# Performance work log

Measured on AMD Instinct MI355X. Metric: run time of the kernel, lower is better.

The kernel has to match this reference:

```python
import jax, jax.numpy as jnp
import numpy as np

N_USERS = 100000
N_ITEMS = 50000
NNZ = 3000000  # user-item interactions; symmetric adjacency has 2*NNZ edges
D = 64
N_LAYERS = 3


def setup_inputs() -> dict:
    key = jax.random.key(0)
    k1, k2, k3 = jax.random.split(key, 3)
    N = N_USERS + N_ITEMS
    users = jax.random.randint(k1, (NNZ,), 0, N_USERS)
    items = jax.random.randint(k2, (NNZ,), 0, N_ITEMS) + N_USERS
    # symmetric bipartite adjacency: u->i and i->u edges
    row = jnp.concatenate([users, items]).astype(jnp.int32)
    col = jnp.concatenate([items, users]).astype(jnp.int32)
    # D^{-1/2} A D^{-1/2} normalization, matching (deg + 1e-7)^{-0.5}
    deg = jax.ops.segment_sum(jnp.ones(row.shape, dtype=jnp.float32), row, num_segments=N)
    dinv = jnp.power(deg + 1e-7, -0.5)
    vals = dinv[row] * dinv[col]
    in_embs = jax.random.normal(k3, (N, D), dtype=jnp.float32)
    return {"in_embs": in_embs, "row": row, "col": col, "vals": vals, "n_layers": N_LAYERS}


def reference(in_embs, row, col, vals, n_layers):
    N = in_embs.shape[0]
    # result = in_embs + sum_i [ x_i/(i+1) + x_i ]  (original appends both per layer)
    out = in_embs
    x = in_embs
    for i in range(n_layers):
        # SpMM: x <- A_norm @ x  via gather + segment scatter-add
        x = jax.ops.segment_sum(vals[:, None] * x[col], row, num_segments=N)
        # F.normalize(x, dim=-1) with torch's eps=1e-12 clamp
        x = x / jnp.maximum(jnp.linalg.norm(x, axis=-1, keepdims=True), 1e-12)
        out = out + x * (1.0 + 1.0 / (i + 1))
    return out
```

## Files before the change

kernel.cpp:

```cpp
#include <hip/hip_runtime.h>
#include <hip/hip_bf16.h>

#define D 64
#define BW 512
#define BSH 9
#define BMASK 511
#define MAXK 512
#define CHUNK 8192

typedef unsigned short u16;
typedef unsigned int u32;
typedef _Float16 half2_t __attribute__((ext_vector_type(2)));

__device__ __forceinline__ u16 f2h(float f) {
    union { _Float16 h; u16 u; } v; v.h = (_Float16)f; return v.u;
}
__device__ __forceinline__ float hlo(u32 u) {
    union { u32 x; half2_t h; } v; v.x = u; return (float)v.h.x;
}
__device__ __forceinline__ float hhi(u32 u) {
    union { u32 x; half2_t h; } v; v.x = u; return (float)v.h.y;
}
__device__ __forceinline__ float dot2lo(u32 u, float acc) {
    union { u32 x; half2_t h; } v; v.x = u;
    half2_t one = {(_Float16)1.0f, (_Float16)0.0f};
    return __builtin_amdgcn_fdot2(v.h, one, acc, false);
}
__device__ __forceinline__ float dot2hi(u32 u, float acc) {
    union { u32 x; half2_t h; } v; v.x = u;
    half2_t one = {(_Float16)0.0f, (_Float16)1.0f};
    return __builtin_amdgcn_fdot2(v.h, one, acc, false);
}


__global__ __launch_bounds__(256) void chunk_hist_kernel(
        const int* __restrict__ row, int* __restrict__ H,
        int E, int K, int nchunks) {
    __shared__ int h[MAXK];
    int ch = blockIdx.x;
    int cbeg = ch * CHUNK;
    int cend = min(cbeg + CHUNK, E);
    for (int i = threadIdx.x; i < K; i += 256) h[i] = 0;
    __syncthreads();
    for (int e = cbeg + threadIdx.x; e < cend; e += 256)
        atomicAdd(&h[row[e] >> BSH], 1);
    __syncthreads();
    for (int i = threadIdx.x; i < K; i += 256)
        H[(size_t)i * nchunks + ch] = h[i];
}


__global__ __launch_bounds__(256) void bucket_colscan_kernel(
        int* __restrict__ H, int* __restrict__ btot, int nchunks) {
    __shared__ int tmp[256];
    int b = blockIdx.x;
    int t = threadIdx.x;
    int* Hb = H + (size_t)b * nchunks;
    int cpt = (nchunks + 255) >> 8;
    int beg = min(t * cpt, nchunks), end = min(beg + cpt, nchunks);
    int s = 0;
    for (int i = beg; i < end; ++i) s += Hb[i];
    tmp[t] = s;
    __syncthreads();
    for (int d = 1; d < 256; d <<= 1) {
        int x = (t >= d) ? tmp[t - d] : 0;
        __syncthreads();
        tmp[t] += x;
        __syncthreads();
    }
    int run = tmp[t] - s;
    for (int i = beg; i < end; ++i) {
        int v = Hb[i];
        Hb[i] = run;
        run += v;
    }
    if (t == 255) btot[b] = tmp[255];
}


__global__ __launch_bounds__(1024) void bucket_scan_kernel(
        const int* __restrict__ btot, int* __restrict__ bbase, int K, int E) {
    __shared__ int tmp[1024];
    int t = threadIdx.x;
    int v = (t < K) ? btot[t] : 0;
    tmp[t] = v;
    __syncthreads();
    for (int d = 1; d < 1024; d <<= 1) {
        int x = (t >= d) ? tmp[t - d] : 0;
        __syncthreads();
        tmp[t] += x;
        __syncthreads();
    }
    if (t < K) bbase[t] = tmp[t] - v;
    if (t == 0) bbase[K] = E;
}


__global__ __launch_bounds__(256) void scatter_sort_kernel(
        const int* __restrict__ row, const int* __restrict__ col,
        const int* __restrict__ H, const int* __restrict__ btot,
        const int* __restrict__ bbase,
        u32* __restrict__ pairs, int E, int K, int nchunks) {
    __shared__ u32 stage[CHUNK];
    __shared__ int hcur[MAXK];
    __shared__ int lbase[MAXK + 1];
    __shared__ int gdest[MAXK];
    __shared__ int red[256];
    int ch = blockIdx.x;
    int cbeg = ch * CHUNK;
    int cend = min(cbeg + CHUNK, E);
    int cnt_total = cend - cbeg;
    int t = threadIdx.x;

    int c0 = 0, c1 = 0;
    int i0 = t, i1 = t + 256;
    if (i0 < K) {
        int st = H[(size_t)i0 * nchunks + ch];
        int en = (ch + 1 < nchunks) ? H[(size_t)i0 * nchunks + ch + 1] : btot[i0];
        c0 = en - st;
        gdest[i0] = bbase[i0] + st;
    }
    if (i1 < K) {
        int st = H[(size_t)i1 * nchunks + ch];
        int en = (ch + 1 < nchunks) ? H[(size_t)i1 * nchunks + ch + 1] : btot[i1];
        c1 = en - st;
        gdest[i1] = bbase[i1] + st;
    }
    __syncthreads();
    int j0 = 2 * t, j1 = 2 * t + 1;
    int d0 = 0, d1 = 0;
    if (j0 < K) {
        int st = H[(size_t)j0 * nchunks + ch];
        int en = (ch + 1 < nchunks) ? H[(size_t)j0 * nchunks + ch + 1] : btot[j0];
        d0 = en - st;
        gdest[j0] = bbase[j0] + st;
    }
    if (j1 < K) {
        int st = H[(size_t)j1 * nchunks + ch];
        int en = (ch + 1 < nchunks) ? H[(size_t)j1 * nchunks + ch + 1] : btot[j1];
        d1 = en - st;
        gdest[j1] = bbase[j1] + st;
    }
    int s = d0 + d1;
    red[t] = s;
    __syncthreads();
    for (int d = 1; d < 256; d <<= 1) {
        int x = (t >= d) ? red[t - d] : 0;
        __syncthreads();
        red[t] += x;
        __syncthreads();
    }
    int ex = red[t] - s;
    if (j0 < K) { lbase[j0] = ex; hcur[j0] = ex; }
    if (j1 < K) { lbase[j1] = ex + d0; hcur[j1] = ex + d0; }
    if (t == 255) lbase[K] = red[255];
    __syncthreads();

    for (int e = cbeg + t; e < cend; e += 256) {
        int r = row[e];
        u32 c = (u32)col[e];
        int p = atomicAdd(&hcur[r >> BSH], 1);
        stage[p] = ((u32)(r & BMASK) << 18) | c;
    }
    __syncthreads();

    for (int p = t; p < cnt_total; p += 256) {
        int lo = 0, hi = K;
        while (hi - lo > 1) {
            int mid = (lo + hi) >> 1;
            if (lbase[mid] <= p) lo = mid; else hi = mid;
        }
        pairs[gdest[lo] + (p - lbase[lo])] = stage[p];
    }
}


__global__ __launch_bounds__(256) void build_csr_kernel(
        const u32* __restrict__ pairs, const int* __restrict__ bbase,
        int* __restrict__ ptr, float* __restrict__ dinv,
        float* __restrict__ sdeg, int* __restrict__ ccol, int N, int K) {
    __shared__ int hd[BW];
    __shared__ int red[256];
    int k = blockIdx.x;
    int ebeg = bbase[k], eend = bbase[k + 1];
    int r0 = k << BSH;
    int t = threadIdx.x;
    hd[t] = 0;
    hd[t + 256] = 0;
    __syncthreads();
    for (int e = ebeg + t; e < eend; e += 256)
        atomicAdd(&hd[pairs[e] >> 18], 1);
    __syncthreads();
    int v0 = hd[2 * t], v1 = hd[2 * t + 1];
    int s = v0 + v1;
    red[t] = s;
    __syncthreads();
    for (int d = 1; d < 256; d <<= 1) {
        int x = (t >= d) ? red[t - d] : 0;
        __syncthreads();
        red[t] += x;
        __syncthreads();
    }
    int ex = red[t] - s;
    int fb0 = ebeg + ex;
    int fb1 = ebeg + ex + v0;
    int ra = r0 + 2 * t, rb = r0 + 2 * t + 1;
    if (ra < N) {
        ptr[ra] = fb0;
        float f = (float)v0 + 1e-7f;
        float sq = sqrtf(f);
        dinv[ra] = 1.0f / sq;
        sdeg[ra] = sq;
    }
    if (rb < N) {
        ptr[rb] = fb1;
        float f = (float)v1 + 1e-7f;
        float sq = sqrtf(f);
        dinv[rb] = 1.0f / sq;
        sdeg[rb] = sq;
    }
    hd[2 * t] = fb0;
    hd[2 * t + 1] = fb1;
    if (k == 0 && t == 0) ptr[N] = eend >= 0 ? bbase[K] : 0;
    __syncthreads();
    for (int e = ebeg + t; e < eend; e += 256) {
        u32 pk = pairs[e];
        int pos = atomicAdd(&hd[pk >> 18], 1);
        ccol[pos] = (int)(pk & 0x3FFFFu);
    }
}

__global__ void scale_in_kernel(const float* __restrict__ in,
                                const float* __restrict__ dinv,
                                u16* __restrict__ y0, int npairs) {
    int p = blockIdx.x * blockDim.x + threadIdx.x;
    if (p >= npairs) return;
    float2 v = *reinterpret_cast<const float2*>(&in[(size_t)p * 2]);
    float dv = dinv[p >> 5];
    u32 up = (u32)f2h(v.x * dv) | ((u32)f2h(v.y * dv) << 16);
    *reinterpret_cast<u32*>(&y0[(size_t)p * 2]) = up;
}

template <bool FINAL>
__global__ __launch_bounds__(256) void layer_kernel(
        const u16* __restrict__ y_src,
        const int* __restrict__ ptr,
        const int* __restrict__ ccol,
        const float* __restrict__ dinv,
        const float* __restrict__ sdeg,
        u16* __restrict__ y_dst,
        const float* __restrict__ in_embs,
        const u16* __restrict__ y1,
        float* __restrict__ out,
        int rbeg, int rend) {
    int wid = (blockIdx.x * blockDim.x + threadIdx.x) >> 6;
    int lane = threadIdx.x & 63;
    int rh = lane >> 5;
    int b = (lane >> 3) & 3;
    int a = lane & 7;
    int r = rbeg + wid * 2 + rh;
    if (r >= rend) return;
    const size_t dimoff = (size_t)a * 8;

    int s = ptr[r], e = ptr[r + 1];
    float acc[8];
    #pragma unroll
    for (int i = 0; i < 8; ++i) acc[i] = 0.f;

#define ACCQ(q)                                            \
    do {                                                   \
        u32 qa_[4] = {(q).x, (q).y, (q).z, (q).w};         \
        _Pragma("unroll")                                  \
        for (int i_ = 0; i_ < 4; ++i_) {                   \
            acc[2 * i_]     = dot2lo(qa_[i_], acc[2 * i_]);     \
            acc[2 * i_ + 1] = dot2hi(qa_[i_], acc[2 * i_ + 1]); \
        }                                                  \
    } while (0)

    int j = s;
    #pragma unroll 2
    for (; j + 8 <= e; j += 8) {
        int c0 = __builtin_nontemporal_load(&ccol[j + b]);
        int c1 = __builtin_nontemporal_load(&ccol[j + 4 + b]);
        uint4 q0 = *reinterpret_cast<const uint4*>(&y_src[(size_t)c0 * D + dimoff]);
        uint4 q1 = *reinterpret_cast<const uint4*>(&y_src[(size_t)c1 * D + dimoff]);
        ACCQ(q0);
        ACCQ(q1);
    }
    if (j + 4 <= e) {
        int c = __builtin_nontemporal_load(&ccol[j + b]);
        uint4 q = *reinterpret_cast<const uint4*>(&y_src[(size_t)c * D + dimoff]);
        ACCQ(q);
        j += 4;
    }
    if (j + b < e) {
        int c = __builtin_nontemporal_load(&ccol[j + b]);
        uint4 q = *reinterpret_cast<const uint4*>(&y_src[(size_t)c * D + dimoff]);
        ACCQ(q);
    }
#undef ACCQ

    #pragma unroll
    for (int off = 8; off <= 16; off <<= 1) {
        #pragma unroll
        for (int i = 0; i < 8; ++i) acc[i] += __shfl_xor(acc[i], off);
    }

    float ss = 0.f;
    #pragma unroll
    for (int i = 0; i < 8; ++i) ss += acc[i] * acc[i];
    #pragma unroll
    for (int off = 1; off <= 4; off <<= 1) ss += __shfl_xor(ss, off);
    float inv = 1.0f / fmaxf(sqrtf(ss), 1e-12f);

    if (b == 0) {
        size_t idx = (size_t)r * D + dimoff;
        if (FINAL) {
            float sd = sdeg[r];
            float4 i0 = *reinterpret_cast<const float4*>(&in_embs[idx]);
            float4 i1 = *reinterpret_cast<const float4*>(&in_embs[idx + 4]);
            uint4 w1 = *reinterpret_cast<const uint4*>(&y1[idx]);
            uint4 w2 = *reinterpret_cast<const uint4*>(&y_src[idx]);
            u32 w1a[4] = {w1.x, w1.y, w1.z, w1.w};
            u32 w2a[4] = {w2.x, w2.y, w2.z, w2.w};
            float o[8];
            #pragma unroll
            for (int i = 0; i < 4; ++i) {
                o[2 * i]     = 2.0f * sd * hlo(w1a[i]) + 1.5f * sd * hlo(w2a[i])
                             + (4.0f / 3.0f) * acc[2 * i] * inv;
                o[2 * i + 1] = 2.0f * sd * hhi(w1a[i]) + 1.5f * sd * hhi(w2a[i])
                             + (4.0f / 3.0f) * acc[2 * i + 1] * inv;
            }
            float4 o0 = {o[0] + i0.x, o[1] + i0.y, o[2] + i0.z, o[3] + i0.w};
            float4 o1 = {o[4] + i1.x, o[5] + i1.y, o[6] + i1.z, o[7] + i1.w};
            *reinterpret_cast<float4*>(&out[idx])     = o0;
            *reinterpret_cast<float4*>(&out[idx + 4]) = o1;
        } else {
            float dv = dinv[r] * inv;
            uint4 w;
            w.x = (u32)f2h(acc[0] * dv) | ((u32)f2h(acc[1] * dv) << 16);
            w.y = (u32)f2h(acc[2] * dv) | ((u32)f2h(acc[3] * dv) << 16);
            w.z = (u32)f2h(acc[4] * dv) | ((u32)f2h(acc[5] * dv) << 16);
            w.w = (u32)f2h(acc[6] * dv) | ((u32)f2h(acc[7] * dv) << 16);
            *reinterpret_cast<uint4*>(&y_dst[idx]) = w;
        }
    }
}


__global__ void spmm_scatter_kernel(const float* __restrict__ x_src,
                                    const int* __restrict__ row,
                                    const int* __restrict__ col,
                                    const float* __restrict__ vals,
                                    float* __restrict__ x_dst, int E) {
    int gid = blockIdx.x * blockDim.x + threadIdx.x;
    int e = gid >> 6;
    int lane = threadIdx.x & 63;
    if (e >= E) return;
    float xv = x_src[(size_t)col[e] * D + lane];
    atomicAdd(&x_dst[(size_t)row[e] * D + lane], vals[e] * xv);
}

__global__ void norm_accum_kernel(float* __restrict__ x, float* __restrict__ out,
                                  float coef, int N) {
    int gid = blockIdx.x * blockDim.x + threadIdx.x;
    int rowi = gid >> 6;
    int lane = threadIdx.x & 63;
    if (rowi >= N) return;
    size_t idx = (size_t)rowi * D + lane;
    float v = x[idx];
    float s = v * v;
    #pragma unroll
    for (int off = 32; off >= 1; off >>= 1) s += __shfl_xor(s, off);
    float nv = v / fmaxf(sqrtf(s), 1e-12f);
    x[idx] = nv;
    out[idx] += coef * nv;
}

static inline size_t align256(size_t x) { return (x + 255) & ~(size_t)255; }

extern "C" void kernel_launch(void* const* d_in, const int* in_sizes, int n_in,
                              void* d_out, int out_size, void* d_ws, size_t ws_size,
                              hipStream_t stream) {
    const float* in_embs = (const float*)d_in[0];
    const int*   row     = (const int*)d_in[1];
    const int*   col     = (const int*)d_in[2];
    const float* vals    = (const float*)d_in[3];

    const int N = in_sizes[0] / D;
    const int E = in_sizes[1];

    float* out = (float*)d_out;

    const size_t embElems = (size_t)N * D;
    const size_t f16Bytes = embElems * sizeof(u16);
    const int K = (N + BW - 1) / BW;
    const int nchunks = (E + CHUNK - 1) / CHUNK;
    const size_t Hbytes = (size_t)K * nchunks * 4;

    size_t off = 0;
    const size_t o_ccol  = off; off += align256((size_t)E * 4);
    const size_t o_ptr   = off; off += align256(((size_t)N + 1) * 4);
    const size_t o_dinv  = off; off += align256((size_t)N * 4);
    const size_t o_sdeg  = off; off += align256((size_t)N * 4);
    const size_t o_btot  = off; off += align256((size_t)MAXK * 4);
    const size_t o_bbase = off; off += align256(((size_t)MAXK + 1) * 4);
    const size_t o_X     = off;
    const size_t xNeedA  = align256((size_t)E * 4) + align256(Hbytes);
    const size_t xNeedB  = 2 * align256(f16Bytes);
    const size_t xBytes  = (xNeedA > xNeedB) ? xNeedA : xNeedB;
    const size_t needed  = o_X + align256(xBytes);

    dim3 block(256);
    const int npairs = (int)(embElems / 2);
    dim3 pgrid((unsigned)((npairs + 255) / 256));

    if (ws_size >= needed && K <= MAXK) {
        char* wsb = (char*)d_ws;
        int*   ccol  = (int*)(wsb + o_ccol);
        int*   ptr   = (int*)(wsb + o_ptr);
        float* dinv  = (float*)(wsb + o_dinv);
        float* sdeg  = (float*)(wsb + o_sdeg);
        int*   btot  = (int*)(wsb + o_btot);
        int*   bbase = (int*)(wsb + o_bbase);
        u32*   pairs = (u32*)(wsb + o_X);
        int*   H     = (int*)(wsb + o_X + align256((size_t)E * 4));
        u16*   bufA  = (u16*)(wsb + o_X);
        u16*   bufB  = (u16*)(wsb + o_X + align256(f16Bytes));

        chunk_hist_kernel<<<dim3((unsigned)nchunks), block, 0, stream>>>(
            row, H, E, K, nchunks);
        bucket_colscan_kernel<<<dim3((unsigned)K), block, 0, stream>>>(
            H, btot, nchunks);
        bucket_scan_kernel<<<dim3(1), dim3(1024), 0, stream>>>(btot, bbase, K, E);
        scatter_sort_kernel<<<dim3((unsigned)nchunks), block, 0, stream>>>(
            row, col, H, btot, bbase, pairs, E, K, nchunks);
        build_csr_kernel<<<dim3((unsigned)K), block, 0, stream>>>(
            pairs, bbase, ptr, dinv, sdeg, ccol, N, K);

        scale_in_kernel<<<pgrid, block, 0, stream>>>(in_embs, dinv, bufA, npairs);

        int nu = (N == 150000) ? 100000 : N;
        auto launch_layer = [&](const u16* src, u16* dst, const u16* y1p,
                                bool fin, int rb, int re) {
            int rows = re - rb;
            if (rows <= 0) return;
            dim3 g((unsigned)(((rows + 1) / 2 + 3) / 4));
            if (fin)
                layer_kernel<true><<<g, block, 0, stream>>>(
                    src, ptr, ccol, dinv, sdeg, nullptr, in_embs, y1p, out, rb, re);
            else
                layer_kernel<false><<<g, block, 0, stream>>>(
                    src, ptr, ccol, dinv, sdeg, dst, nullptr, nullptr, nullptr, rb, re);
        };

        launch_layer(bufA, bufB, nullptr, false, 0, nu);
        launch_layer(bufA, bufB, nullptr, false, nu, N);
        launch_layer(bufB, bufA, nullptr, false, 0, nu);
        launch_layer(bufB, bufA, nullptr, false, nu, N);
        launch_layer(bufA, nullptr, bufB, true, 0, nu);
        launch_layer(bufA, nullptr, bufB, true, nu, N);
    } else {
        float* fA = (float*)d_ws;
        float* fB = fA + embElems;
        hipMemcpyAsync(out, in_embs, embElems * 4, hipMemcpyDeviceToDevice, stream);
        const float coefs[3] = {2.0f, 1.5f, 4.0f / 3.0f};
        dim3 sgrid((unsigned)((E + 3) / 4));
        dim3 ngrid((unsigned)((N + 3) / 4));
        const float* src = in_embs;
        float* dst = fA;
        float* other = fB;
        for (int i = 0; i < 3; ++i) {
            hipMemsetAsync(dst, 0, embElems * 4, stream);
            spmm_scatter_kernel<<<sgrid, block, 0, stream>>>(src, row, col, vals, dst, E);
            norm_accum_kernel<<<ngrid, block, 0, stream>>>(dst, out, coefs[i], N);
            src = dst;
            float* t = dst; dst = other; other = t;
        }
    }
}
```

Before: 464.2 us.

## Split CSR build into hist, scan and fill kernels across bucket sub-ranges

Replaces the single build_csr kernel, which used one block per 512-row bucket (about 293 blocks), with three kernels. Each bucket's edge range is split into 8 slices: per-slice histograms are computed, scanned per bucket into per-slice offsets, and a fill kernel then scatters columns, with the block index swizzled so a bucket's slices share an XCD. The aim is more parallelism in the CSR build, at the cost of two extra launches and an extra P buffer round trip. It also removes a redundant H read block in scatter_sort and uses a nontemporal load for row in the histogram.

```diff
diff --git a/kernel.cpp b/kernel.cpp
--- a/kernel.cpp
+++ b/kernel.cpp
@@ -7,6 +7,7 @@
 #define BMASK 511
 #define MAXK 512
 #define CHUNK 8192
+#define SSPLIT 8
 
 typedef unsigned short u16;
 typedef unsigned int u32;
@@ -43,7 +44,7 @@
     for (int i = threadIdx.x; i < K; i += 256) h[i] = 0;
     __syncthreads();
     for (int e = cbeg + threadIdx.x; e < cend; e += 256)
-        atomicAdd(&h[row[e] >> BSH], 1);
+        atomicAdd(&h[__builtin_nontemporal_load(&row[e]) >> BSH], 1);
     __syncthreads();
     for (int i = threadIdx.x; i < K; i += 256)
         H[(size_t)i * nchunks + ch] = h[i];
@@ -112,21 +113,6 @@
     int cnt_total = cend - cbeg;
     int t = threadIdx.x;
 
-    int c0 = 0, c1 = 0;
-    int i0 = t, i1 = t + 256;
-    if (i0 < K) {
-        int st = H[(size_t)i0 * nchunks + ch];
-        int en = (ch + 1 < nchunks) ? H[(size_t)i0 * nchunks + ch + 1] : btot[i0];
-        c0 = en - st;
-        gdest[i0] = bbase[i0] + st;
-    }
-    if (i1 < K) {
-        int st = H[(size_t)i1 * nchunks + ch];
-        int en = (ch + 1 < nchunks) ? H[(size_t)i1 * nchunks + ch + 1] : btot[i1];
-        c1 = en - st;
-        gdest[i1] = bbase[i1] + st;
-    }
-    __syncthreads();
     int j0 = 2 * t, j1 = 2 * t + 1;
     int d0 = 0, d1 = 0;
     if (j0 < K) {
@@ -175,25 +161,45 @@
 }
 
 
-__global__ __launch_bounds__(256) void build_csr_kernel(
+__global__ __launch_bounds__(256) void csr_hist_kernel(
         const u32* __restrict__ pairs, const int* __restrict__ bbase,
+        int* __restrict__ P, int K) {
+    __shared__ int h[BW];
+    int b = blockIdx.x;
+    int k = b / SSPLIT, s = b % SSPLIT;
+    int t = threadIdx.x;
+    h[t] = 0; h[t + 256] = 0;
+    __syncthreads();
+    int ebeg = bbase[k], eend = bbase[k + 1];
+    int len = eend - ebeg;
+    int sb = ebeg + (int)((long long)len * s / SSPLIT);
+    int se = ebeg + (int)((long long)len * (s + 1) / SSPLIT);
+    for (int e = sb + t; e < se; e += 256)
+        atomicAdd(&h[pairs[e] >> 18], 1);
+    __syncthreads();
+    int* Pks = P + ((size_t)k * SSPLIT + s) * BW;
+    Pks[t] = h[t];
+    Pks[t + 256] = h[t + 256];
+}
+
+__global__ __launch_bounds__(256) void csr_scan_kernel(
+        int* __restrict__ P, const int* __restrict__ bbase,
         int* __restrict__ ptr, float* __restrict__ dinv,
-        float* __restrict__ sdeg, int* __restrict__ ccol, int N, int K) {
-    __shared__ int hd[BW];
+        float* __restrict__ sdeg, int N, int K) {
     __shared__ int red[256];
     int k = blockIdx.x;
-    int ebeg = bbase[k], eend = bbase[k + 1];
+    int t = threadIdx.x;
     int r0 = k << BSH;
-    int t = threadIdx.x;
-    hd[t] = 0;
-    hd[t + 256] = 0;
-    __syncthreads();
-    for (int e = ebeg + t; e < eend; e += 256)
-        atomicAdd(&hd[pairs[e] >> 18], 1);
-    __syncthreads();
-    int v0 = hd[2 * t], v1 = hd[2 * t + 1];
-    int s = v0 + v1;
-    red[t] = s;
+    int* Pk = P + (size_t)k * SSPLIT * BW;
+    int q0[SSPLIT], q1[SSPLIT];
+    int d0 = 0, d1 = 0;
+    #pragma unroll
+    for (int s = 0; s < SSPLIT; ++s) {
+        q0[s] = d0; d0 += Pk[s * BW + 2 * t];
+        q1[s] = d1; d1 += Pk[s * BW + 2 * t + 1];
+    }
+    int sum = d0 + d1;
+    red[t] = sum;
     __syncthreads();
     for (int d = 1; d < 256; d <<= 1) {
         int x = (t >= d) ? red[t - d] : 0;
@@ -201,31 +207,55 @@
         red[t] += x;
         __syncthreads();
     }
-    int ex = red[t] - s;
-    int fb0 = ebeg + ex;
-    int fb1 = ebeg + ex + v0;
+    int ex = red[t] - sum;
+    int base0 = bbase[k] + ex;
+    int base1 = base0 + d0;
     int ra = r0 + 2 * t, rb = r0 + 2 * t + 1;
     if (ra < N) {
-        ptr[ra] = fb0;
-        float f = (float)v0 + 1e-7f;
+        ptr[ra] = base0;
+        float f = (float)d0 + 1e-7f;
         float sq = sqrtf(f);
         dinv[ra] = 1.0f / sq;
         sdeg[ra] = sq;
     }
     if (rb < N) {
-        ptr[rb] = fb1;
-        float f = (float)v1 + 1e-7f;
+        ptr[rb] = base1;
+        float f = (float)d1 + 1e-7f;
         float sq = sqrtf(f);
         dinv[rb] = 1.0f / sq;
         sdeg[rb] = sq;
     }
-    hd[2 * t] = fb0;
-    hd[2 * t + 1] = fb1;
-    if (k == 0 && t == 0) ptr[N] = eend >= 0 ? bbase[K] : 0;
-    __syncthreads();
-    for (int e = ebeg + t; e < eend; e += 256) {
+    #pragma unroll
+    for (int s = 0; s < SSPLIT; ++s) {
+        Pk[s * BW + 2 * t]     = base0 + q0[s];
+        Pk[s * BW + 2 * t + 1] = base1 + q1[s];
+    }
+    if (k == 0 && t == 0) ptr[N] = bbase[K];
+}
+
+__global__ __launch_bounds__(256) void csr_fill_kernel(
+        const u32* __restrict__ pairs, const int* __restrict__ bbase,
+        const int* __restrict__ P, int* __restrict__ ccol, int K) {
+    __shared__ int cur[BW];
+    int b = blockIdx.x;
+    int xcd = b & 7;
+    int q = b >> 3;
+    int s = q % SSPLIT;
+    int kk = q / SSPLIT;
+    int k = kk * 8 + xcd;
+    if (k >= K) return;
+    int t = threadIdx.x;
+    const int* Pks = P + ((size_t)k * SSPLIT + s) * BW;
+    cur[t] = Pks[t];
+    cur[t + 256] = Pks[t + 256];
+    __syncthreads();
+    int ebeg = bbase[k], eend = bbase[k + 1];
+    int len = eend - ebeg;
+    int sb = ebeg + (int)((long long)len * s / SSPLIT);
+    int se = ebeg + (int)((long long)len * (s + 1) / SSPLIT);
+    for (int e = sb + t; e < se; e += 256) {
         u32 pk = pairs[e];
-        int pos = atomicAdd(&hd[pk >> 18], 1);
+        int pos = atomicAdd(&cur[pk >> 18], 1);
         ccol[pos] = (int)(pk & 0x3FFFFu);
     }
 }
@@ -397,6 +427,7 @@
     const int K = (N + BW - 1) / BW;
     const int nchunks = (E + CHUNK - 1) / CHUNK;
     const size_t Hbytes = (size_t)K * nchunks * 4;
+    const size_t Pbytes = (size_t)K * SSPLIT * BW * 4;
 
     size_t off = 0;
     const size_t o_ccol  = off; off += align256((size_t)E * 4);
@@ -406,7 +437,7 @@
     const size_t o_btot  = off; off += align256((size_t)MAXK * 4);
     const size_t o_bbase = off; off += align256(((size_t)MAXK + 1) * 4);
     const size_t o_X     = off;
-    const size_t xNeedA  = align256((size_t)E * 4) + align256(Hbytes);
+    const size_t xNeedA  = align256((size_t)E * 4) + align256(Hbytes) + align256(Pbytes);
     const size_t xNeedB  = 2 * align256(f16Bytes);
     const size_t xBytes  = (xNeedA > xNeedB) ? xNeedA : xNeedB;
     const size_t needed  = o_X + align256(xBytes);
@@ -425,6 +456,7 @@
         int*   bbase = (int*)(wsb + o_bbase);
         u32*   pairs = (u32*)(wsb + o_X);
         int*   H     = (int*)(wsb + o_X + align256((size_t)E * 4));
+        int*   P     = (int*)(wsb + o_X + align256((size_t)E * 4) + align256(Hbytes));
         u16*   bufA  = (u16*)(wsb + o_X);
         u16*   bufB  = (u16*)(wsb + o_X + align256(f16Bytes));
 
@@ -435,8 +467,13 @@
         bucket_scan_kernel<<<dim3(1), dim3(1024), 0, stream>>>(btot, bbase, K, E);
         scatter_sort_kernel<<<dim3((unsigned)nchunks), block, 0, stream>>>(
             row, col, H, btot, bbase, pairs, E, K, nchunks);
-        build_csr_kernel<<<dim3((unsigned)K), block, 0, stream>>>(
-            pairs, bbase, ptr, dinv, sdeg, ccol, N, K);
+        csr_hist_kernel<<<dim3((unsigned)(K * SSPLIT)), block, 0, stream>>>(
+            pairs, bbase, P, K);
+        csr_scan_kernel<<<dim3((unsigned)K), block, 0, stream>>>(
+            P, bbase, ptr, dinv, sdeg, N, K);
+        const unsigned fillGrid = 8u * SSPLIT * ((K + 7) / 8);
+        csr_fill_kernel<<<dim3(fillGrid), block, 0, stream>>>(
+            pairs, bbase, P, ccol, K);
 
         scale_in_kernel<<<pgrid, block, 0, stream>>>(in_embs, dinv, bufA, npairs);
 
```

Measured after the change: 433.1 us. 6.7% less time.
